# Kernel optimization log

Measured on AMD Instinct MI355X. Metric: run time of the kernel, lower is better.

## Reference

```python
import jax, jax.numpy as jnp
import numpy as np

KERNEL_SIZE = 3

def setup_inputs() -> dict:
    key = jax.random.key(0)
    k1, k2, k3, k4, k5 = jax.random.split(key, 5)
    B, L, D, K = 4, 4096, 1024, KERNEL_SIZE
    x = jax.random.normal(k1, (B, L, D), dtype=jnp.float32)
    # depthwise conv: torch weight shape (D, 1, K) -> store as (D, K)
    fan_dw = 1.0 / np.sqrt(1 * K)
    w_dw = jax.random.uniform(k2, (D, K), dtype=jnp.float32, minval=-fan_dw, maxval=fan_dw)
    b_dw = jax.random.uniform(k3, (D,), dtype=jnp.float32, minval=-fan_dw, maxval=fan_dw)
    # pointwise conv: torch weight shape (D, D, 1) -> store as (D_out, D_in)
    fan_pw = 1.0 / np.sqrt(D * 1)
    w_pw = jax.random.uniform(k4, (D, D), dtype=jnp.float32, minval=-fan_pw, maxval=fan_pw)
    b_pw = jax.random.uniform(k5, (D,), dtype=jnp.float32, minval=-fan_pw, maxval=fan_pw)
    return {"x": x, "w_dw": w_dw, "b_dw": b_dw, "w_pw": w_pw, "b_pw": b_pw}

def _causal_dw_pw(x, w_dw, b_dw, w_pw, b_pw):
    # x: (B, L, D); causal left-pad by K-1 along L
    K = w_dw.shape[1]
    L = x.shape[1]
    xp = jnp.pad(x, ((0, 0), (K - 1, 0), (0, 0)))  # (B, L+K-1, D)
    # depthwise: y[b,l,d] = sum_k xp[b,l+k,d] * w_dw[d,k]
    y = sum(xp[:, k:k + L, :] * w_dw[:, k] for k in range(K)) + b_dw
    # pointwise 1x1 conv: mix channels
    return jnp.einsum('bld,ed->ble', y, w_pw) + b_pw

def reference(x, w_dw, b_dw, w_pw, b_pw):
    return _causal_dw_pw(x, w_dw, b_dw, w_pw, b_pw)
```

## Files before the change

kernel.cpp:

```cpp
#include <hip/hip_runtime.h>
#include <hip/hip_bf16.h>
#include <stdint.h>

#define B_SZ   4
#define L_SEQ  4096
#define D_DIM  1024
#define M_TOT  (B_SZ * L_SEQ)

typedef __bf16 bf16;
typedef __attribute__((ext_vector_type(8))) __bf16 bf16x8;
typedef __attribute__((ext_vector_type(4))) float   f32x4;

#define GLOAD_LDS16(g, l)                                                     \
  __builtin_amdgcn_global_load_lds(                                           \
      (const __attribute__((address_space(1))) void*)(g),                     \
      (__attribute__((address_space(3))) void*)(l), 16, 0, 0)

__global__ __launch_bounds__(256) void dw_bf16_kernel(
    const float* __restrict__ x, const float* __restrict__ w_dw,
    const float* __restrict__ b_dw, bf16* __restrict__ y,
    const float* __restrict__ w_pw, bf16* __restrict__ wpwb) {
  const int t = threadIdx.x;
  if (blockIdx.x >= B_SZ * (L_SEQ / 16)) {
    int i = ((blockIdx.x - B_SZ * (L_SEQ / 16)) * 256 + t) * 8;
    float4 a = *(const float4*)(w_pw + i);
    float4 b = *(const float4*)(w_pw + i + 4);
    union { bf16 h[8]; int4 v; } r;
    r.h[0] = (bf16)a.x; r.h[1] = (bf16)a.y; r.h[2] = (bf16)a.z; r.h[3] = (bf16)a.w;
    r.h[4] = (bf16)b.x; r.h[5] = (bf16)b.y; r.h[6] = (bf16)b.z; r.h[7] = (bf16)b.w;
    *(int4*)(wpwb + i) = r.v;
    return;
  }
  const int b  = blockIdx.x >> 8;
  const int l0 = (blockIdx.x & 255) * 16;
  const int d0 = t * 4;
  const float* xb = x + (size_t)b * L_SEQ * D_DIM + d0;
  bf16*        yb = y + (size_t)b * L_SEQ * D_DIM + d0;

  float4 xr[18];
  const float4 zero = make_float4(0.f, 0.f, 0.f, 0.f);
  xr[0] = (l0 >= 2) ? *(const float4*)(xb + (size_t)(l0 - 2) * D_DIM) : zero;
  xr[1] = (l0 >= 1) ? *(const float4*)(xb + (size_t)(l0 - 1) * D_DIM) : zero;
#pragma unroll
  for (int j = 0; j < 16; ++j)
    xr[j + 2] = *(const float4*)(xb + (size_t)(l0 + j) * D_DIM);

  const float* wp = w_dw + d0 * 3;
  float4 wa = *(const float4*)(wp);
  float4 wb = *(const float4*)(wp + 4);
  float4 wc = *(const float4*)(wp + 8);
  float4 bv = *(const float4*)(b_dw + d0);

#pragma unroll
  for (int j = 0; j < 16; ++j) {
    float4 x2 = xr[j], x1 = xr[j + 1], x0 = xr[j + 2];
    float a0 = fmaf(x2.x, wa.x, fmaf(x1.x, wa.y, fmaf(x0.x, wa.z, bv.x)));
    float a1 = fmaf(x2.y, wa.w, fmaf(x1.y, wb.x, fmaf(x0.y, wb.y, bv.y)));
    float a2 = fmaf(x2.z, wb.z, fmaf(x1.z, wb.w, fmaf(x0.z, wc.x, bv.z)));
    float a3 = fmaf(x2.w, wc.y, fmaf(x1.w, wc.z, fmaf(x0.w, wc.w, bv.w)));
    union { bf16 h[4]; int2 v; } o;
    o.h[0] = (bf16)a0; o.h[1] = (bf16)a1; o.h[2] = (bf16)a2; o.h[3] = (bf16)a3;
    *(int2*)(yb + (size_t)(l0 + j) * D_DIM) = o.v;
  }
}

#define EP_ROWP 68

__global__ __launch_bounds__(512, 2) void gemm256_kernel(
    const bf16* __restrict__ A,
    const bf16* __restrict__ Bm,
    const float* __restrict__ bias, float* __restrict__ C) {
  __shared__ __align__(16) char smem[131072];

  const int t    = threadIdx.x;
  const int m0   = blockIdx.x * 256;
  const int n0   = blockIdx.y * 256;
  const int lane = t & 63;
  const int wv   = t >> 6;
  const int wmh  = wv >> 2;
  const int wn   = wv & 3;
  const int lrow = lane & 15;
  const int q    = lane >> 4;

  unsigned ra[8], rb[4];
#pragma unroll
  for (int i = 0; i < 8; ++i) {
    int row = wmh * 128 + i * 16 + lrow;
    unsigned a = (unsigned)(row * 64) +
                 ((((unsigned)q) ^ ((unsigned)((row >> 1) & 3))) << 4);
    a ^= ((unsigned)((row >> 2) & 1)) << 6;
    ra[i] = a;
  }
#pragma unroll
  for (int j = 0; j < 4; ++j) {
    int row = wn * 64 + j * 16 + lrow;
    unsigned a = (unsigned)(row * 64) +
                 ((((unsigned)q) ^ ((unsigned)((row >> 1) & 3))) << 4);
    a ^= ((unsigned)((row >> 2) & 1)) << 6;
    rb[j] = a;
  }

  const bf16* agp[2];
  const bf16* bgp[2];
#pragma unroll
  for (int r = 0; r < 2; ++r) {
    int rs = r * 128 + (t >> 2);
    int grow = rs ^ ((rs >> 2) & 1);
    int gc   = (t & 3) ^ ((rs >> 1) & 3);
    agp[r] = A  + (size_t)(m0 + grow) * D_DIM + gc * 8;
    bgp[r] = Bm + (size_t)(n0 + grow) * D_DIM + gc * 8;
  }
  const unsigned lbase = (unsigned)(wv * 1024);

  auto stageA = [&](int kt) {
    unsigned bb = (unsigned)((kt & 3) * 32768);
#pragma unroll
    for (int r = 0; r < 2; ++r)
      GLOAD_LDS16(agp[r] + kt * 32, smem + bb + r * 8192 + lbase);
  };
  auto stageB = [&](int kt) {
    unsigned bb = (unsigned)((kt & 3) * 32768 + 16384);
#pragma unroll
    for (int r = 0; r < 2; ++r)
      GLOAD_LDS16(bgp[r] + kt * 32, smem + bb + r * 8192 + lbase);
  };

  f32x4 acc[8][4] = {};

  stageA(0); stageB(0);
  stageA(1); stageB(1);
  stageA(2); stageB(2);

  for (int kt = 0; kt < 32; ++kt) {
    if (kt < 30)       asm volatile("s_waitcnt vmcnt(8)" ::: "memory");
    else if (kt == 30) asm volatile("s_waitcnt vmcnt(4)" ::: "memory");
    else               asm volatile("s_waitcnt vmcnt(0)" ::: "memory");
    __builtin_amdgcn_s_barrier();

    const char* Ab = smem + (size_t)((kt & 3) * 32768);
    const char* Bb = Ab + 16384;

    bf16x8 af[4], bfr[4], af2[4];
#pragma unroll
    for (int i = 0; i < 4; ++i) af[i]  = *(const bf16x8*)(Ab + ra[i]);
#pragma unroll
    for (int j = 0; j < 4; ++j) bfr[j] = *(const bf16x8*)(Bb + rb[j]);
    if (kt <= 28) stageA(kt + 3);
    __builtin_amdgcn_sched_barrier(0);
    __builtin_amdgcn_s_barrier();
    __builtin_amdgcn_s_setprio(1);
#pragma unroll
    for (int i = 0; i < 4; ++i)
#pragma unroll
      for (int j = 0; j < 4; ++j)
        acc[i][j] = __builtin_amdgcn_mfma_f32_16x16x32_bf16(af[i], bfr[j], acc[i][j], 0, 0, 0);
    __builtin_amdgcn_s_setprio(0);
    __builtin_amdgcn_sched_barrier(0);
    __builtin_amdgcn_s_barrier();

#pragma unroll
    for (int i = 0; i < 4; ++i) af2[i] = *(const bf16x8*)(Ab + ra[4 + i]);
    if (kt <= 28) stageB(kt + 3);
    __builtin_amdgcn_sched_barrier(0);
    __builtin_amdgcn_s_barrier();
    __builtin_amdgcn_s_setprio(1);
#pragma unroll
    for (int i = 0; i < 4; ++i)
#pragma unroll
      for (int j = 0; j < 4; ++j)
        acc[4 + i][j] = __builtin_amdgcn_mfma_f32_16x16x32_bf16(af2[i], bfr[j], acc[4 + i][j], 0, 0, 0);
    __builtin_amdgcn_s_setprio(0);
  }

  float* ep = (float*)smem + (size_t)wv * (16 * EP_ROWP);

  float bvj[4];
#pragma unroll
  for (int j = 0; j < 4; ++j) bvj[j] = bias[n0 + wn * 64 + j * 16 + lrow];

#pragma unroll
  for (int i = 0; i < 8; ++i) {
#pragma unroll
    for (int j = 0; j < 4; ++j)
#pragma unroll
      for (int r = 0; r < 4; ++r)
        ep[(q * 4 + r) * EP_ROWP + j * 16 + lrow] = acc[i][j][r] + bvj[j];
#pragma unroll
    for (int it2 = 0; it2 < 4; ++it2) {
      int flat = it2 * 64 + lane;
      int row  = flat >> 4;
      int c16  = flat & 15;
      float4 v = *(const float4*)(ep + row * EP_ROWP + c16 * 4);
      int gm = m0 + wmh * 128 + i * 16 + row;
      int gn = n0 + wn * 64 + c16 * 4;
      *(float4*)(C + (size_t)gm * D_DIM + gn) = v;
    }
  }
}

__global__ __launch_bounds__(256) void fallback_kernel(
    const float* __restrict__ x, const float* __restrict__ w_dw,
    const float* __restrict__ b_dw, const float* __restrict__ w_pw,
    const float* __restrict__ b_pw, float* __restrict__ out) {
  __shared__ float ys[D_DIM];
  const int m = blockIdx.x;
  const int l = m & (L_SEQ - 1);
  const int t = threadIdx.x;
  const float* xr = x + (size_t)m * D_DIM;
#pragma unroll
  for (int c = 0; c < 4; ++c) {
    int d = t + c * 256;
    float a = fmaf(xr[d], w_dw[d * 3 + 2], b_dw[d]);
    if (l >= 1) a = fmaf(xr[d - D_DIM], w_dw[d * 3 + 1], a);
    if (l >= 2) a = fmaf(xr[d - 2 * D_DIM], w_dw[d * 3 + 0], a);
    ys[d] = a;
  }
  __syncthreads();
#pragma unroll
  for (int c = 0; c < 4; ++c) {
    int e = t + c * 256;
    const float* wr = w_pw + (size_t)e * D_DIM;
    float a = b_pw[e];
    for (int d = 0; d < D_DIM; ++d) a = fmaf(ys[d], wr[d], a);
    out[(size_t)m * D_DIM + e] = a;
  }
}

extern "C" void kernel_launch(void* const* d_in, const int* in_sizes, int n_in,
                              void* d_out, int out_size, void* d_ws, size_t ws_size,
                              hipStream_t stream) {
  (void)in_sizes; (void)n_in; (void)out_size;
  const float* x    = (const float*)d_in[0];
  const float* w_dw = (const float*)d_in[1];
  const float* b_dw = (const float*)d_in[2];
  const float* w_pw = (const float*)d_in[3];
  const float* b_pw = (const float*)d_in[4];
  float* out = (float*)d_out;

  const size_t y_elems = (size_t)M_TOT * D_DIM;
  const size_t w_elems = (size_t)D_DIM * D_DIM;
  const size_t need = (y_elems + w_elems) * sizeof(bf16);

  if (ws_size >= need) {
    bf16* y    = (bf16*)d_ws;
    bf16* wpwb = (bf16*)d_ws + y_elems;
    const int dw_blocks  = B_SZ * (L_SEQ / 16);
    const int cvt_blocks = (D_DIM * D_DIM / 8) / 256;
    dw_bf16_kernel<<<dw_blocks + cvt_blocks, 256, 0, stream>>>(x, w_dw, b_dw, y, w_pw, wpwb);
    dim3 grid(M_TOT / 256, D_DIM / 256);
    gemm256_kernel<<<grid, 512, 0, stream>>>(y, wpwb, b_pw, out);
  } else {
    fallback_kernel<<<M_TOT, 256, 0, stream>>>(x, w_dw, b_dw, w_pw, b_pw, out);
  }
}
```

Measured before the change: 155.4 us.

## Merge GEMM k-step into single barrier phase with unified A/B staging

Restructures the GEMM main loop so each k-step has one barrier instead of three. All eight A fragments and four B fragments are read together, then 32 MFMAs are issued in a single prioritized block. A and B tiles now go to separate LDS halves and are staged together per step. The LDS swizzle drops the row-level XOR term, and address setup is reduced to base-plus-stride offsets. In exchange, more fragments are held in registers and the LDS access pattern changes, which may add bank conflicts.

```diff
diff --git a/kernel.cpp b/kernel.cpp
--- a/kernel.cpp
+++ b/kernel.cpp
@@ -65,6 +65,9 @@
 }
 
 #define EP_ROWP 68
+#define SB  __builtin_amdgcn_s_barrier()
+#define SCB __builtin_amdgcn_sched_barrier(0)
+#define VM(N) asm volatile("s_waitcnt vmcnt(" #N ")" ::: "memory")
 
 __global__ __launch_bounds__(512, 2) void gemm256_kernel(
     const bf16* __restrict__ A,
@@ -82,95 +85,53 @@
   const int lrow = lane & 15;
   const int q    = lane >> 4;
 
-  unsigned ra[8], rb[4];
-#pragma unroll
-  for (int i = 0; i < 8; ++i) {
-    int row = wmh * 128 + i * 16 + lrow;
-    unsigned a = (unsigned)(row * 64) +
-                 ((((unsigned)q) ^ ((unsigned)((row >> 1) & 3))) << 4);
-    a ^= ((unsigned)((row >> 2) & 1)) << 6;
-    ra[i] = a;
-  }
-#pragma unroll
-  for (int j = 0; j < 4; ++j) {
-    int row = wn * 64 + j * 16 + lrow;
-    unsigned a = (unsigned)(row * 64) +
-                 ((((unsigned)q) ^ ((unsigned)((row >> 1) & 3))) << 4);
-    a ^= ((unsigned)((row >> 2) & 1)) << 6;
-    rb[j] = a;
-  }
-
-  const bf16* agp[2];
-  const bf16* bgp[2];
-#pragma unroll
-  for (int r = 0; r < 2; ++r) {
-    int rs = r * 128 + (t >> 2);
-    int grow = rs ^ ((rs >> 2) & 1);
-    int gc   = (t & 3) ^ ((rs >> 1) & 3);
-    agp[r] = A  + (size_t)(m0 + grow) * D_DIM + gc * 8;
-    bgp[r] = Bm + (size_t)(n0 + grow) * D_DIM + gc * 8;
-  }
-  const unsigned lbase = (unsigned)(wv * 1024);
-
-  auto stageA = [&](int kt) {
-    unsigned bb = (unsigned)((kt & 3) * 32768);
-#pragma unroll
-    for (int r = 0; r < 2; ++r)
-      GLOAD_LDS16(agp[r] + kt * 32, smem + bb + r * 8192 + lbase);
+  const unsigned cx    = (((unsigned)q ^ (((unsigned)lrow >> 1) & 3)) << 4);
+  const unsigned baseA = (unsigned)((wmh * 128 + lrow) * 64) + cx;
+  const unsigned baseB = (unsigned)((wn * 64 + lrow) * 64) + cx;
+
+  const int grow = t >> 2;
+  const int gc   = (t & 3) ^ ((grow >> 1) & 3);
+  const bf16* aSrc = A  + (size_t)(m0 + grow) * D_DIM + gc * 8;
+  const bf16* bSrc = Bm + (size_t)(n0 + grow) * D_DIM + gc * 8;
+  const unsigned wbase = (unsigned)(wv * 1024);
+
+  auto stage = [&](int s) {
+    const size_t k0 = (size_t)s * 32;
+    unsigned as_ = (unsigned)((s & 3) * 16384) + wbase;
+    GLOAD_LDS16(aSrc + k0,                          smem + as_);
+    GLOAD_LDS16(aSrc + k0 + (size_t)128 * D_DIM,    smem + as_ + 8192);
+    GLOAD_LDS16(bSrc + k0,                          smem + as_ + 65536);
+    GLOAD_LDS16(bSrc + k0 + (size_t)128 * D_DIM,    smem + as_ + 65536 + 8192);
   };
-  auto stageB = [&](int kt) {
-    unsigned bb = (unsigned)((kt & 3) * 32768 + 16384);
-#pragma unroll
-    for (int r = 0; r < 2; ++r)
-      GLOAD_LDS16(bgp[r] + kt * 32, smem + bb + r * 8192 + lbase);
+
+  f32x4 acc[8][4] = {};
+
+  auto body = [&](int s, bool do_stage) {
+    SB;
+    const char* Ab = smem + (size_t)((s & 3) * 16384);
+    const char* Bb = Ab + 65536;
+    bf16x8 bf4[4], af[8];
+#pragma unroll
+    for (int j = 0; j < 4; ++j) bf4[j] = *(const bf16x8*)(Bb + baseB + j * 1024);
+#pragma unroll
+    for (int i = 0; i < 8; ++i) af[i]  = *(const bf16x8*)(Ab + baseA + i * 1024);
+    if (do_stage) stage(s + 3);
+    SCB;
+    __builtin_amdgcn_s_setprio(1);
+#pragma unroll
+    for (int i = 0; i < 8; ++i)
+#pragma unroll
+      for (int j = 0; j < 4; ++j)
+        acc[i][j] = __builtin_amdgcn_mfma_f32_16x16x32_bf16(af[i], bf4[j], acc[i][j], 0, 0, 0);
+    __builtin_amdgcn_s_setprio(0);
+    SCB;
   };
 
-  f32x4 acc[8][4] = {};
-
-  stageA(0); stageB(0);
-  stageA(1); stageB(1);
-  stageA(2); stageB(2);
-
-  for (int kt = 0; kt < 32; ++kt) {
-    if (kt < 30)       asm volatile("s_waitcnt vmcnt(8)" ::: "memory");
-    else if (kt == 30) asm volatile("s_waitcnt vmcnt(4)" ::: "memory");
-    else               asm volatile("s_waitcnt vmcnt(0)" ::: "memory");
-    __builtin_amdgcn_s_barrier();
-
-    const char* Ab = smem + (size_t)((kt & 3) * 32768);
-    const char* Bb = Ab + 16384;
-
-    bf16x8 af[4], bfr[4], af2[4];
-#pragma unroll
-    for (int i = 0; i < 4; ++i) af[i]  = *(const bf16x8*)(Ab + ra[i]);
-#pragma unroll
-    for (int j = 0; j < 4; ++j) bfr[j] = *(const bf16x8*)(Bb + rb[j]);
-    if (kt <= 28) stageA(kt + 3);
-    __builtin_amdgcn_sched_barrier(0);
-    __builtin_amdgcn_s_barrier();
-    __builtin_amdgcn_s_setprio(1);
-#pragma unroll
-    for (int i = 0; i < 4; ++i)
-#pragma unroll
-      for (int j = 0; j < 4; ++j)
-        acc[i][j] = __builtin_amdgcn_mfma_f32_16x16x32_bf16(af[i], bfr[j], acc[i][j], 0, 0, 0);
-    __builtin_amdgcn_s_setprio(0);
-    __builtin_amdgcn_sched_barrier(0);
-    __builtin_amdgcn_s_barrier();
-
-#pragma unroll
-    for (int i = 0; i < 4; ++i) af2[i] = *(const bf16x8*)(Ab + ra[4 + i]);
-    if (kt <= 28) stageB(kt + 3);
-    __builtin_amdgcn_sched_barrier(0);
-    __builtin_amdgcn_s_barrier();
-    __builtin_amdgcn_s_setprio(1);
-#pragma unroll
-    for (int i = 0; i < 4; ++i)
-#pragma unroll
-      for (int j = 0; j < 4; ++j)
-        acc[4 + i][j] = __builtin_amdgcn_mfma_f32_16x16x32_bf16(af2[i], bfr[j], acc[4 + i][j], 0, 0, 0);
-    __builtin_amdgcn_s_setprio(0);
-  }
+  stage(0); stage(1); stage(2);
+
+  for (int s = 0; s < 30; ++s) { VM(8); body(s, s < 29); }
+  VM(4); body(30, false);
+  VM(0); body(31, false);
 
   float* ep = (float*)smem + (size_t)wv * (16 * EP_ROWP);
 
```

Measured after the change: 156.6 us. No clear change (+0.8%).
